# Kernel tuning notes

Hardware: AMD Instinct MI355X
Metric: run time of the kernel (lower is better)

## Reference

```python
import jax, jax.numpy as jnp
import numpy as np

B, T, C, H = 4, 2048, 768, 12
D = C // H

def setup_inputs() -> dict:
    key = jax.random.key(0)
    ks = jax.random.split(key, 8)
    s = 1.0 / np.sqrt(C)
    return {
        "x":  jax.random.normal(ks[0], (B, T, C), dtype=jnp.float32),
        "Wq": jax.random.normal(ks[1], (C, C), dtype=jnp.float32) * s,
        "bq": jax.random.normal(ks[2], (C,), dtype=jnp.float32) * 0.02,
        "Wk": jax.random.normal(ks[3], (C, C), dtype=jnp.float32) * s,
        "bk": jax.random.normal(ks[4], (C,), dtype=jnp.float32) * 0.02,
        "Wv": jax.random.normal(ks[5], (C, C), dtype=jnp.float32) * s,
        "bv": jax.random.normal(ks[6], (C,), dtype=jnp.float32) * 0.02,
        "Wp": jax.random.normal(ks[7], (C, C), dtype=jnp.float32) * s,
    }

def reference(x, Wq, bq, Wk, bk, Wv, bv, Wp):
    # Linear projections (torch Linear: y = x @ W.T + b)
    q = x @ Wq.T + bq
    k = x @ Wk.T + bk
    v = x @ Wv.T + bv
    # [B,T,C] -> [B,H,T,D]
    q = q.reshape(B, T, H, D).transpose(0, 2, 1, 3)
    k = k.reshape(B, T, H, D).transpose(0, 2, 1, 3)
    v = v.reshape(B, T, H, D).transpose(0, 2, 1, 3)
    scale = 1.0 / np.sqrt(D).astype(np.float32)
    scores = jnp.einsum('bhqd,bhkd->bhqk', q, k) * scale  # [B,H,T,T]
    attn = jax.nn.softmax(scores, axis=-1)  # no mask in original module
    out = jnp.einsum('bhqk,bhkd->bhqd', attn, v)
    out = out.transpose(0, 2, 1, 3).reshape(B, T, C)
    return out @ Wp.T  # proj has bias=False
```

## Files before the change

kernel.cpp:

```cpp
#include <hip/hip_runtime.h>
#include <hip/hip_bf16.h>
#include <cmath>

constexpr int B  = 4;
constexpr int T  = 2048;
constexpr int C  = 768;
constexpr int H  = 12;
constexpr int Dh = 64;
constexpr int M  = B * T;
constexpr int NQKV = 3 * C;
constexpr int WS2  = C * C;

typedef short bf16x8 __attribute__((ext_vector_type(8)));
typedef short bf16x4 __attribute__((ext_vector_type(4)));
typedef float f32x4  __attribute__((ext_vector_type(4)));

__device__ inline short f2bf(float f) {
    unsigned u = __float_as_uint(f);
    u += 0x7fffu + ((u >> 16) & 1u);
    return (short)(u >> 16);
}

__device__ inline unsigned pk_bf16(float a, float b) {
    __hip_bfloat162 h = __float22bfloat162_rn(float2{a, b});
    return *(unsigned*)&h;
}

typedef const __attribute__((address_space(1))) unsigned GU;
typedef __attribute__((address_space(3))) unsigned LU;
__device__ inline void async_copy16(const void* g, void* l) {
    __builtin_amdgcn_global_load_lds((GU*)g, (LU*)l, 16, 0, 0);
}

constexpr size_t XE = (size_t)M * C;
constexpr size_t CV_TOTAL = XE + 4 * (size_t)WS2;

__global__ __launch_bounds__(256)
void convert_all(const float* __restrict__ x,  const float* __restrict__ Wq,
                 const float* __restrict__ Wk, const float* __restrict__ Wv,
                 const float* __restrict__ Wp,
                 short* __restrict__ xb, short* __restrict__ Wqkv,
                 short* __restrict__ Wpb) {
    size_t i = ((size_t)blockIdx.x * 256 + threadIdx.x) * 4;
    const float* src; short* dst; size_t off;
    if (i < XE)                        { src = x;  dst = xb;            off = i; }
    else if (i < XE + WS2)             { src = Wq; dst = Wqkv;          off = i - XE; }
    else if (i < XE + 2 * (size_t)WS2) { src = Wk; dst = Wqkv + WS2;    off = i - XE - WS2; }
    else if (i < XE + 3 * (size_t)WS2) { src = Wv; dst = Wqkv + 2 * WS2; off = i - XE - 2 * (size_t)WS2; }
    else                               { src = Wp; dst = Wpb;           off = i - XE - 3 * (size_t)WS2; }
    float4 v = *(const float4*)(src + off);
    bf16x4 o; o[0] = f2bf(v.x); o[1] = f2bf(v.y); o[2] = f2bf(v.z); o[3] = f2bf(v.w);
    *(bf16x4*)(dst + off) = o;
}

constexpr int BM = 128;

template<int BN_, int WMW, int WNW, int OUT_BF16>
__global__ __launch_bounds__(256)
void gemm_bt(const short* __restrict__ A, const short* __restrict__ W,
             const float* __restrict__ bias0, const float* __restrict__ bias1,
             const float* __restrict__ bias2,
             void* __restrict__ Yv, int Ndim, int Kdim) {
    constexpr int MT  = BM / WMW / 16;
    constexpr int NT  = BN_ / WNW / 16;
    constexpr int NCH = (BM + BN_) / 16;

    __shared__ short As[2][BM * 32];
    __shared__ short Bs[2][BN_ * 32];

    const int tid  = threadIdx.x;
    const int wave = tid >> 6;
    const int lane = tid & 63;
    const int li   = lane & 15;
    const int quad = lane >> 4;
    const int wm   = wave % WMW;
    const int wn   = wave / WMW;
    const int m0   = blockIdx.y * BM;
    const int n0   = blockIdx.x * BN_;

    f32x4 acc[MT][NT];
    #pragma unroll
    for (int i = 0; i < MT; ++i)
        #pragma unroll
        for (int j = 0; j < NT; ++j)
            acc[i][j] = (f32x4){0.f, 0.f, 0.f, 0.f};

    const int lrow = lane >> 2;
    const int lkof = (lane & 3) * 8;

    for (int k0 = 0; k0 < Kdim; k0 += 64) {
        __syncthreads();
        #pragma unroll
        for (int h = 0; h < 2; ++h)
            #pragma unroll
            for (int ii = 0; ii < NCH / 4; ++ii) {
                int c = ii * 4 + wave;
                if (c < BM / 16)
                    async_copy16(A + (size_t)(m0 + c * 16 + lrow) * Kdim
                                   + k0 + h * 32 + lkof,
                                 &As[h][c * 512]);
                else
                    async_copy16(W + (size_t)(n0 + (c - BM / 16) * 16 + lrow) * Kdim
                                   + k0 + h * 32 + lkof,
                                 &Bs[h][(c - BM / 16) * 512]);
            }
        __syncthreads();

        #pragma unroll
        for (int h = 0; h < 2; ++h) {
            bf16x8 af[MT], bfr[NT];
            #pragma unroll
            for (int t = 0; t < MT; ++t)
                af[t] = *(const bf16x8*)&As[h][(wm * MT * 16 + t * 16 + li) * 32 + quad * 8];
            #pragma unroll
            for (int t = 0; t < NT; ++t)
                bfr[t] = *(const bf16x8*)&Bs[h][(wn * NT * 16 + t * 16 + li) * 32 + quad * 8];
            #pragma unroll
            for (int i = 0; i < MT; ++i)
                #pragma unroll
                for (int j = 0; j < NT; ++j)
                    acc[i][j] = __builtin_amdgcn_mfma_f32_16x16x32_bf16(
                        af[i], bfr[j], acc[i][j], 0, 0, 0);
        }
    }

    float bb[NT];
    #pragma unroll
    for (int nt = 0; nt < NT; ++nt) bb[nt] = 0.f;
    if (bias0) {
        int s = n0 / C;
        const float* bp = (s == 0) ? bias0 : ((s == 1) ? bias1 : bias2);
        int nb = n0 % C;
        #pragma unroll
        for (int nt = 0; nt < NT; ++nt)
            bb[nt] = bp[nb + wn * NT * 16 + nt * 16 + li];
    }

    #pragma unroll
    for (int mt = 0; mt < MT; ++mt)
        #pragma unroll
        for (int nt = 0; nt < NT; ++nt)
            #pragma unroll
            for (int r = 0; r < 4; ++r) {
                int row = m0 + wm * MT * 16 + mt * 16 + quad * 4 + r;
                int col = n0 + wn * NT * 16 + nt * 16 + li;
                float v = acc[mt][nt][r] + bb[nt];
                if constexpr (OUT_BF16)
                    ((short*)Yv)[(size_t)row * Ndim + col] = f2bf(v);
                else
                    ((float*)Yv)[(size_t)row * Ndim + col] = v;
            }
}

constexpr int QT   = 128;
constexpr int KTT  = 64;
constexpr int LSTR = 72;
constexpr int PSTR = 72;
constexpr int QS   = NQKV;
constexpr float SOFT_SCALE = 0.18033688011112042f;

__global__ __launch_bounds__(256)
void attn_fwd(const short* __restrict__ QKV, short* __restrict__ O) {
    __shared__ short Ks[KTT * LSTR];
    __shared__ short Vt[Dh * LSTR];
    __shared__ short Ps[4 * 32 * PSTR];

    const int tid  = threadIdx.x;
    const int wave = tid >> 6;
    const int lane = tid & 63;
    const int li   = lane & 15;
    const int quad = lane >> 4;
    const int b    = blockIdx.z;
    const int h    = blockIdx.y;
    const int qw   = blockIdx.x * QT + wave * 32;

    const short* Qg = QKV + (size_t)(b * T) * QS + h * Dh;
    const short* Kg = QKV + (size_t)(b * T) * QS + C + h * Dh;
    const short* Vg = QKV + (size_t)(b * T) * QS + 2 * C + h * Dh;

    bf16x8 qf[2][2];
    #pragma unroll
    for (int qb = 0; qb < 2; ++qb)
        #pragma unroll
        for (int dh = 0; dh < 2; ++dh)
            qf[qb][dh] = *(const bf16x8*)(Qg + (size_t)(qw + qb * 16 + li) * QS
                                             + dh * 32 + quad * 8);

    bf16x8 ones;
    #pragma unroll
    for (int i = 0; i < 8; ++i) ones[i] = (short)0x3F80;

    f32x4 oacc[2][4];
    #pragma unroll
    for (int qb = 0; qb < 2; ++qb)
        #pragma unroll
        for (int db = 0; db < 4; ++db)
            oacc[qb][db] = (f32x4){0.f, 0.f, 0.f, 0.f};
    f32x4 lacc[2] = {(f32x4){0.f, 0.f, 0.f, 0.f}, (f32x4){0.f, 0.f, 0.f, 0.f}};

    const int ktok = tid >> 3;
    const int kch  = tid & 7;
    const int vd2  = (tid & 31) * 2;
    const int vg   = tid >> 5;

    int4 kpre[2];
    unsigned vpre[8];
    kpre[0] = *(const int4*)(Kg + (size_t)(ktok)      * QS + kch * 8);
    kpre[1] = *(const int4*)(Kg + (size_t)(ktok + 32) * QS + kch * 8);
    #pragma unroll
    for (int t2 = 0; t2 < 8; ++t2)
        vpre[t2] = *(const unsigned*)(Vg + (size_t)(vg * 8 + t2) * QS + vd2);

    for (int kt = 0; kt < T; kt += KTT) {
        __syncthreads();

        *(int4*)&Ks[ktok * LSTR + kch * 8]        = kpre[0];
        *(int4*)&Ks[(ktok + 32) * LSTR + kch * 8] = kpre[1];
        {
            unsigned lo[4], hi[4];
            #pragma unroll
            for (int j = 0; j < 4; ++j) {
                lo[j] = __builtin_amdgcn_perm(vpre[2 * j + 1], vpre[2 * j], 0x05040100u);
                hi[j] = __builtin_amdgcn_perm(vpre[2 * j + 1], vpre[2 * j], 0x07060302u);
            }
            *(int4*)&Vt[vd2 * LSTR + vg * 8]       = make_int4(lo[0], lo[1], lo[2], lo[3]);
            *(int4*)&Vt[(vd2 + 1) * LSTR + vg * 8] = make_int4(hi[0], hi[1], hi[2], hi[3]);
        }
        __syncthreads();

        if (kt + KTT < T) {
            const size_t nb = kt + KTT;
            kpre[0] = *(const int4*)(Kg + (nb + ktok)      * QS + kch * 8);
            kpre[1] = *(const int4*)(Kg + (nb + ktok + 32) * QS + kch * 8);
            #pragma unroll
            for (int t2 = 0; t2 < 8; ++t2)
                vpre[t2] = *(const unsigned*)(Vg + (nb + vg * 8 + t2) * QS + vd2);
        }

        f32x4 st[2][4];
        #pragma unroll
        for (int kb = 0; kb < 4; ++kb) {
            bf16x8 kf0 = *(const bf16x8*)&Ks[(kb * 16 + li) * LSTR + quad * 8];
            bf16x8 kf1 = *(const bf16x8*)&Ks[(kb * 16 + li) * LSTR + 32 + quad * 8];
            #pragma unroll
            for (int qb = 0; qb < 2; ++qb) {
                f32x4 a = (f32x4){0.f, 0.f, 0.f, 0.f};
                a = __builtin_amdgcn_mfma_f32_16x16x32_bf16(kf0, qf[qb][0], a, 0, 0, 0);
                a = __builtin_amdgcn_mfma_f32_16x16x32_bf16(kf1, qf[qb][1], a, 0, 0, 0);
                st[qb][kb] = a;
            }
        }

        #pragma unroll
        for (int qb = 0; qb < 2; ++qb)
            #pragma unroll
            for (int kb = 0; kb < 4; ++kb) {
                float p0 = __builtin_amdgcn_exp2f(st[qb][kb][0] * SOFT_SCALE);
                float p1 = __builtin_amdgcn_exp2f(st[qb][kb][1] * SOFT_SCALE);
                float p2 = __builtin_amdgcn_exp2f(st[qb][kb][2] * SOFT_SCALE);
                float p3 = __builtin_amdgcn_exp2f(st[qb][kb][3] * SOFT_SCALE);
                uint2 w; w.x = pk_bf16(p0, p1); w.y = pk_bf16(p2, p3);
                *(uint2*)&Ps[(wave * 32 + qb * 16 + li) * PSTR + kb * 16 + quad * 4] = w;
            }
        __asm__ volatile("s_waitcnt lgkmcnt(0)" ::: "memory");

        #pragma unroll
        for (int kq = 0; kq < 2; ++kq) {
            bf16x8 pf[2];
            #pragma unroll
            for (int qb = 0; qb < 2; ++qb) {
                pf[qb] = *(const bf16x8*)&Ps[(wave * 32 + qb * 16 + li) * PSTR
                                             + kq * 32 + quad * 8];
                lacc[qb] = __builtin_amdgcn_mfma_f32_16x16x32_bf16(
                    pf[qb], ones, lacc[qb], 0, 0, 0);
            }
            #pragma unroll
            for (int db = 0; db < 4; ++db) {
                bf16x8 vf = *(const bf16x8*)&Vt[(db * 16 + li) * LSTR + kq * 32 + quad * 8];
                #pragma unroll
                for (int qb = 0; qb < 2; ++qb)
                    oacc[qb][db] = __builtin_amdgcn_mfma_f32_16x16x32_bf16(
                        pf[qb], vf, oacc[qb][db], 0, 0, 0);
            }
        }
    }

    #pragma unroll
    for (int qb = 0; qb < 2; ++qb)
        #pragma unroll
        for (int r = 0; r < 4; ++r) {
            float inv = 1.0f / lacc[qb][r];
            short* op = O + (size_t)(b * T + qw + qb * 16 + quad * 4 + r) * C
                          + h * Dh + li;
            #pragma unroll
            for (int db = 0; db < 4; ++db)
                op[db * 16] = f2bf(oacc[qb][db][r] * inv);
        }
}

extern "C" void kernel_launch(void* const* d_in, const int* in_sizes, int n_in,
                              void* d_out, int out_size, void* d_ws, size_t ws_size,
                              hipStream_t stream) {
    (void)in_sizes; (void)n_in; (void)out_size; (void)ws_size;

    const float* x  = (const float*)d_in[0];
    const float* Wq = (const float*)d_in[1];
    const float* bq = (const float*)d_in[2];
    const float* Wk = (const float*)d_in[3];
    const float* bk = (const float*)d_in[4];
    const float* Wv = (const float*)d_in[5];
    const float* bv = (const float*)d_in[6];
    const float* Wp = (const float*)d_in[7];
    float* out = (float*)d_out;

    short* xb    = (short*)d_ws;
    short* Wqkv  = xb + (size_t)M * C;
    short* Wpb   = Wqkv + 3 * (size_t)WS2;
    short* QKVb  = Wpb + (size_t)WS2;
    short* AOb   = QKVb + (size_t)M * NQKV;

    convert_all<<<dim3(CV_TOTAL / 1024), 256, 0, stream>>>(
        x, Wq, Wk, Wv, Wp, xb, Wqkv, Wpb);

    gemm_bt<128, 2, 2, 1><<<dim3(NQKV / 128, M / BM), 256, 0, stream>>>(
        xb, Wqkv, bq, bk, bv, QKVb, NQKV, C);

    attn_fwd<<<dim3(T / QT, H, B), 256, 0, stream>>>(QKVb, AOb);

    gemm_bt<64, 4, 1, 0><<<dim3(C / 64, M / BM), 256, 0, stream>>>(
        AOb, Wpb, nullptr, nullptr, nullptr, out, C, C);
}
```

Measured before the change: 240.2 us.

## Use 32x32 MFMA in attention with register-resident P via permlane swaps

The attention kernel moves from 16x16x32 to 32x32x16 MFMA tiles, so each wave computes its 32 queries against the 64-key tile as two 32x32 score blocks. The probabilities are repacked in registers with permlane32_swap instead of going through a shared-memory P buffer, which removes LDS traffic and a wait. The softmax scale is folded into the Q projection GEMM epilogue, s_setprio is raised around the MFMA bursts, and launch bounds request three blocks per SM. Applying the scale to bf16 Q before the product changes rounding slightly. The larger accumulator fragments may also raise register pressure.

```diff
diff --git a/kernel.cpp b/kernel.cpp
--- a/kernel.cpp
+++ b/kernel.cpp
@@ -14,6 +14,9 @@
 typedef short bf16x8 __attribute__((ext_vector_type(8)));
 typedef short bf16x4 __attribute__((ext_vector_type(4)));
 typedef float f32x4  __attribute__((ext_vector_type(4)));
+typedef float f32x16 __attribute__((ext_vector_type(16)));
+
+constexpr float SOFT_SCALE = 0.18033688011112042f;
 
 __device__ inline short f2bf(float f) {
     unsigned u = __float_as_uint(f);
@@ -24,6 +27,12 @@
 __device__ inline unsigned pk_bf16(float a, float b) {
     __hip_bfloat162 h = __float22bfloat162_rn(float2{a, b});
     return *(unsigned*)&h;
+}
+
+__device__ inline bf16x8 mk8(unsigned a, unsigned b, unsigned c, unsigned d) {
+    union { unsigned u[4]; bf16x8 v; } x;
+    x.u[0] = a; x.u[1] = b; x.u[2] = c; x.u[3] = d;
+    return x.v;
 }
 
 typedef const __attribute__((address_space(1))) unsigned GU;
@@ -55,7 +64,7 @@
 
 constexpr int BM = 128;
 
-template<int BN_, int WMW, int WNW, int OUT_BF16>
+template<int BN_, int WMW, int WNW, int OUT_BF16, int QSCALE>
 __global__ __launch_bounds__(256)
 void gemm_bt(const short* __restrict__ A, const short* __restrict__ W,
              const float* __restrict__ bias0, const float* __restrict__ bias1,
@@ -145,6 +154,9 @@
                 int row = m0 + wm * MT * 16 + mt * 16 + quad * 4 + r;
                 int col = n0 + wn * NT * 16 + nt * 16 + li;
                 float v = acc[mt][nt][r] + bb[nt];
+                if constexpr (QSCALE) {
+                    if (n0 < C) v *= SOFT_SCALE;
+                }
                 if constexpr (OUT_BF16)
                     ((short*)Yv)[(size_t)row * Ndim + col] = f2bf(v);
                 else
@@ -155,21 +167,18 @@
 constexpr int QT   = 128;
 constexpr int KTT  = 64;
 constexpr int LSTR = 72;
-constexpr int PSTR = 72;
 constexpr int QS   = NQKV;
-constexpr float SOFT_SCALE = 0.18033688011112042f;
-
-__global__ __launch_bounds__(256)
+
+__global__ __launch_bounds__(256, 3)
 void attn_fwd(const short* __restrict__ QKV, short* __restrict__ O) {
     __shared__ short Ks[KTT * LSTR];
     __shared__ short Vt[Dh * LSTR];
-    __shared__ short Ps[4 * 32 * PSTR];
 
     const int tid  = threadIdx.x;
     const int wave = tid >> 6;
     const int lane = tid & 63;
-    const int li   = lane & 15;
-    const int quad = lane >> 4;
+    const int r31  = lane & 31;
+    const int hi   = lane >> 5;
     const int b    = blockIdx.z;
     const int h    = blockIdx.y;
     const int qw   = blockIdx.x * QT + wave * 32;
@@ -178,25 +187,18 @@
     const short* Kg = QKV + (size_t)(b * T) * QS + C + h * Dh;
     const short* Vg = QKV + (size_t)(b * T) * QS + 2 * C + h * Dh;
 
-    bf16x8 qf[2][2];
-    #pragma unroll
-    for (int qb = 0; qb < 2; ++qb)
-        #pragma unroll
-        for (int dh = 0; dh < 2; ++dh)
-            qf[qb][dh] = *(const bf16x8*)(Qg + (size_t)(qw + qb * 16 + li) * QS
-                                             + dh * 32 + quad * 8);
+    bf16x8 qf[4];
+    #pragma unroll
+    for (int f = 0; f < 4; ++f)
+        qf[f] = *(const bf16x8*)(Qg + (size_t)(qw + r31) * QS + f * 16 + hi * 8);
 
     bf16x8 ones;
     #pragma unroll
     for (int i = 0; i < 8; ++i) ones[i] = (short)0x3F80;
 
-    f32x4 oacc[2][4];
-    #pragma unroll
-    for (int qb = 0; qb < 2; ++qb)
-        #pragma unroll
-        for (int db = 0; db < 4; ++db)
-            oacc[qb][db] = (f32x4){0.f, 0.f, 0.f, 0.f};
-    f32x4 lacc[2] = {(f32x4){0.f, 0.f, 0.f, 0.f}, (f32x4){0.f, 0.f, 0.f, 0.f}};
+    f32x16 oacc0 = (f32x16)(0.f);
+    f32x16 oacc1 = (f32x16)(0.f);
+    f32x16 lacc  = (f32x16)(0.f);
 
     const int ktok = tid >> 3;
     const int kch  = tid & 7;
@@ -217,14 +219,14 @@
         *(int4*)&Ks[ktok * LSTR + kch * 8]        = kpre[0];
         *(int4*)&Ks[(ktok + 32) * LSTR + kch * 8] = kpre[1];
         {
-            unsigned lo[4], hi[4];
+            unsigned lo[4], hh[4];
             #pragma unroll
             for (int j = 0; j < 4; ++j) {
                 lo[j] = __builtin_amdgcn_perm(vpre[2 * j + 1], vpre[2 * j], 0x05040100u);
-                hi[j] = __builtin_amdgcn_perm(vpre[2 * j + 1], vpre[2 * j], 0x07060302u);
+                hh[j] = __builtin_amdgcn_perm(vpre[2 * j + 1], vpre[2 * j], 0x07060302u);
             }
             *(int4*)&Vt[vd2 * LSTR + vg * 8]       = make_int4(lo[0], lo[1], lo[2], lo[3]);
-            *(int4*)&Vt[(vd2 + 1) * LSTR + vg * 8] = make_int4(hi[0], hi[1], hi[2], hi[3]);
+            *(int4*)&Vt[(vd2 + 1) * LSTR + vg * 8] = make_int4(hh[0], hh[1], hh[2], hh[3]);
         }
         __syncthreads();
 
@@ -237,65 +239,59 @@
                 vpre[t2] = *(const unsigned*)(Vg + (nb + vg * 8 + t2) * QS + vd2);
         }
 
-        f32x4 st[2][4];
-        #pragma unroll
-        for (int kb = 0; kb < 4; ++kb) {
-            bf16x8 kf0 = *(const bf16x8*)&Ks[(kb * 16 + li) * LSTR + quad * 8];
-            bf16x8 kf1 = *(const bf16x8*)&Ks[(kb * 16 + li) * LSTR + 32 + quad * 8];
-            #pragma unroll
-            for (int qb = 0; qb < 2; ++qb) {
-                f32x4 a = (f32x4){0.f, 0.f, 0.f, 0.f};
-                a = __builtin_amdgcn_mfma_f32_16x16x32_bf16(kf0, qf[qb][0], a, 0, 0, 0);
-                a = __builtin_amdgcn_mfma_f32_16x16x32_bf16(kf1, qf[qb][1], a, 0, 0, 0);
-                st[qb][kb] = a;
+        f32x16 st0 = (f32x16)(0.f);
+        f32x16 st1 = (f32x16)(0.f);
+        __builtin_amdgcn_s_setprio(1);
+        #pragma unroll
+        for (int f = 0; f < 4; ++f) {
+            bf16x8 k0 = *(const bf16x8*)&Ks[(r31)      * LSTR + f * 16 + hi * 8];
+            bf16x8 k1 = *(const bf16x8*)&Ks[(32 + r31) * LSTR + f * 16 + hi * 8];
+            st0 = __builtin_amdgcn_mfma_f32_32x32x16_bf16(k0, qf[f], st0, 0, 0, 0);
+            st1 = __builtin_amdgcn_mfma_f32_32x32x16_bf16(k1, qf[f], st1, 0, 0, 0);
+        }
+        __builtin_amdgcn_s_setprio(0);
+
+        #pragma unroll
+        for (int kb = 0; kb < 2; ++kb) {
+            f32x16 s = kb ? st1 : st0;
+            unsigned d[8];
+            #pragma unroll
+            for (int j = 0; j < 8; ++j) {
+                float pa = __builtin_amdgcn_exp2f(s[2 * j]);
+                float pb = __builtin_amdgcn_exp2f(s[2 * j + 1]);
+                d[j] = pk_bf16(pa, pb);
             }
-        }
-
-        #pragma unroll
-        for (int qb = 0; qb < 2; ++qb)
-            #pragma unroll
-            for (int kb = 0; kb < 4; ++kb) {
-                float p0 = __builtin_amdgcn_exp2f(st[qb][kb][0] * SOFT_SCALE);
-                float p1 = __builtin_amdgcn_exp2f(st[qb][kb][1] * SOFT_SCALE);
-                float p2 = __builtin_amdgcn_exp2f(st[qb][kb][2] * SOFT_SCALE);
-                float p3 = __builtin_amdgcn_exp2f(st[qb][kb][3] * SOFT_SCALE);
-                uint2 w; w.x = pk_bf16(p0, p1); w.y = pk_bf16(p2, p3);
-                *(uint2*)&Ps[(wave * 32 + qb * 16 + li) * PSTR + kb * 16 + quad * 4] = w;
-            }
-        __asm__ volatile("s_waitcnt lgkmcnt(0)" ::: "memory");
-
-        #pragma unroll
-        for (int kq = 0; kq < 2; ++kq) {
-            bf16x8 pf[2];
-            #pragma unroll
-            for (int qb = 0; qb < 2; ++qb) {
-                pf[qb] = *(const bf16x8*)&Ps[(wave * 32 + qb * 16 + li) * PSTR
-                                             + kq * 32 + quad * 8];
-                lacc[qb] = __builtin_amdgcn_mfma_f32_16x16x32_bf16(
-                    pf[qb], ones, lacc[qb], 0, 0, 0);
-            }
-            #pragma unroll
-            for (int db = 0; db < 4; ++db) {
-                bf16x8 vf = *(const bf16x8*)&Vt[(db * 16 + li) * LSTR + kq * 32 + quad * 8];
-                #pragma unroll
-                for (int qb = 0; qb < 2; ++qb)
-                    oacc[qb][db] = __builtin_amdgcn_mfma_f32_16x16x32_bf16(
-                        pf[qb], vf, oacc[qb][db], 0, 0, 0);
-            }
+            auto s02 = __builtin_amdgcn_permlane32_swap(d[0], d[2], false, false);
+            auto s13 = __builtin_amdgcn_permlane32_swap(d[1], d[3], false, false);
+            auto s46 = __builtin_amdgcn_permlane32_swap(d[4], d[6], false, false);
+            auto s57 = __builtin_amdgcn_permlane32_swap(d[5], d[7], false, false);
+            bf16x8 pf0 = mk8(s02[0], s13[0], s02[1], s13[1]);
+            bf16x8 pf1 = mk8(s46[0], s57[0], s46[1], s57[1]);
+
+            __builtin_amdgcn_s_setprio(1);
+            lacc = __builtin_amdgcn_mfma_f32_32x32x16_bf16(pf0, ones, lacc, 0, 0, 0);
+            lacc = __builtin_amdgcn_mfma_f32_32x32x16_bf16(pf1, ones, lacc, 0, 0, 0);
+
+            bf16x8 v00 = *(const bf16x8*)&Vt[(r31)      * LSTR + kb * 32 + hi * 8];
+            bf16x8 v01 = *(const bf16x8*)&Vt[(r31)      * LSTR + kb * 32 + 16 + hi * 8];
+            bf16x8 v10 = *(const bf16x8*)&Vt[(32 + r31) * LSTR + kb * 32 + hi * 8];
+            bf16x8 v11 = *(const bf16x8*)&Vt[(32 + r31) * LSTR + kb * 32 + 16 + hi * 8];
+            oacc0 = __builtin_amdgcn_mfma_f32_32x32x16_bf16(pf0, v00, oacc0, 0, 0, 0);
+            oacc0 = __builtin_amdgcn_mfma_f32_32x32x16_bf16(pf1, v01, oacc0, 0, 0, 0);
+            oacc1 = __builtin_amdgcn_mfma_f32_32x32x16_bf16(pf0, v10, oacc1, 0, 0, 0);
+            oacc1 = __builtin_amdgcn_mfma_f32_32x32x16_bf16(pf1, v11, oacc1, 0, 0, 0);
+            __builtin_amdgcn_s_setprio(0);
         }
     }
 
     #pragma unroll
-    for (int qb = 0; qb < 2; ++qb)
-        #pragma unroll
-        for (int r = 0; r < 4; ++r) {
-            float inv = 1.0f / lacc[qb][r];
-            short* op = O + (size_t)(b * T + qw + qb * 16 + quad * 4 + r) * C
-                          + h * Dh + li;
-            #pragma unroll
-            for (int db = 0; db < 4; ++db)
-                op[db * 16] = f2bf(oacc[qb][db][r] * inv);
-        }
+    for (int r = 0; r < 16; ++r) {
+        float inv = 1.0f / lacc[r];
+        int row = (r & 3) + 8 * (r >> 2) + 4 * hi;
+        short* op = O + (size_t)(b * T + qw + row) * C + h * Dh + r31;
+        op[0]  = f2bf(oacc0[r] * inv);
+        op[32] = f2bf(oacc1[r] * inv);
+    }
 }
 
 extern "C" void kernel_launch(void* const* d_in, const int* in_sizes, int n_in,
@@ -322,11 +318,11 @@
     convert_all<<<dim3(CV_TOTAL / 1024), 256, 0, stream>>>(
         x, Wq, Wk, Wv, Wp, xb, Wqkv, Wpb);
 
-    gemm_bt<128, 2, 2, 1><<<dim3(NQKV / 128, M / BM), 256, 0, stream>>>(
+    gemm_bt<128, 2, 2, 1, 1><<<dim3(NQKV / 128, M / BM), 256, 0, stream>>>(
         xb, Wqkv, bq, bk, bv, QKVb, NQKV, C);
 
     attn_fwd<<<dim3(T / QT, H, B), 256, 0, stream>>>(QKVb, AOb);
 
-    gemm_bt<64, 4, 1, 0><<<dim3(C / 64, M / BM), 256, 0, stream>>>(
+    gemm_bt<64, 4, 1, 0, 0><<<dim3(C / 64, M / BM), 256, 0, stream>>>(
         AOb, Wpb, nullptr, nullptr, nullptr, out, C, C);
 }
```

Result: no change. 236.3 us (-1.6%).
